# Optimization experiments

Measured on AMD Instinct MI355X. Metric: run time of the kernel, lower is better.

The kernel has to match this reference:

```python
import jax, jax.numpy as jnp
import numpy as np
import itertools

N_OBJECTS = 6  # subsets of range(6), sizes 1..6 -> 63 subsets

def _subset_groups():
    # group subsets by length so each group runs as one batched LSTM
    groups = {}
    for m in range(1, N_OBJECTS + 1):
        for s in itertools.combinations(range(6), m):
            groups.setdefault(m, []).append(list(s))
    return [(m, np.asarray(v, dtype=np.int32)) for m, v in groups.items()]

SUBSET_GROUPS = _subset_groups()


def _lstm_final_h(x, W_ih, W_hh, b_ih, b_hh):
    """x: [B,T,D] -> final hidden state [B,H]. PyTorch gate order i,f,g,o."""
    H = W_hh.shape[1]
    B = x.shape[0]
    # precompute input projections for all timesteps: [B,T,4H]
    xz = jnp.einsum('btd,gd->btg', x, W_ih) + b_ih + b_hh

    def step(carry, xt):
        h, c = carry
        z = xt + h @ W_hh.T
        i, f, g, o = jnp.split(z, 4, axis=-1)
        c = jax.nn.sigmoid(f) * c + jax.nn.sigmoid(i) * jnp.tanh(g)
        h = jax.nn.sigmoid(o) * jnp.tanh(c)
        return (h, c), None

    h0 = jnp.zeros((B, H), x.dtype)
    (h, _), _ = jax.lax.scan(step, (h0, h0), jnp.swapaxes(xz, 0, 1))
    return h


def setup_inputs() -> dict:
    key = jax.random.key(0)
    ks = jax.random.split(key, 10)
    D, H, FC, A = 16, 128, 256, 10
    mb = 8192
    s = lambda k, shape, fan: jax.random.normal(k, shape, jnp.float32) * (1.0 / np.sqrt(fan))
    return {
        'x_input': jax.random.normal(ks[0], (mb, 6, D), jnp.float32),
        'W_ih': s(ks[1], (4 * H, D), D),
        'W_hh': s(ks[2], (4 * H, H), H),
        'b_ih': jnp.zeros((4 * H,), jnp.float32),
        'b_hh': jnp.zeros((4 * H,), jnp.float32),
        'fc1_W': s(ks[3], (FC, H), H),
        'fc1_b': jnp.zeros((FC,), jnp.float32),
        'fc2_W': s(ks[4], (A, FC), FC),
        'fc2_b': jnp.zeros((A,), jnp.float32),
    }


def reference(x_input, W_ih, W_hh, b_ih, b_hh, fc1_W, fc1_b, fc2_W, fc2_b):
    mb = x_input.shape[0]
    H = W_hh.shape[1]
    hs = []
    # subsets of the same length are batched into one LSTM pass (fused form of
    # the original 63-iteration python loop); aggregation is permutation-invariant
    for m, idx in SUBSET_GROUPS:
        nL = idx.shape[0]
        xg = x_input[:, idx, :]                       # [mb, nL, m, D] gather
        xg = xg.reshape(mb * nL, m, x_input.shape[-1])
        h = _lstm_final_h(xg, W_ih, W_hh, b_ih, b_hh)  # [mb*nL, H]
        hs.append(h.reshape(mb, nL, H))
    holder = jnp.concatenate(hs, axis=1)              # [mb, 63, H]
    x = jnp.max(holder, axis=1)                       # aggregate == 'max'
    x = jax.nn.relu(x @ fc1_W.T + fc1_b)
    x = x @ fc2_W.T + fc2_b
    return jax.nn.log_softmax(x, axis=-1)
```

## Files before the change

kernel.cpp:

```cpp
#include <hip/hip_runtime.h>
#include <hip/hip_bf16.h>

#define BLOCK   512
#define NSAMP   32
#define HDIM    128
#define DDIM    16
#define NOBJ    6
#define NSLOT   16

typedef __attribute__((ext_vector_type(8))) short bf16x8;
typedef __attribute__((ext_vector_type(4))) float f32x4;

constexpr int pc6(int m)  { int c = 0; for (int i = 0; i < 6; ++i) c += (m >> i) & 1; return c; }
constexpr int msb6(int m) { int b = -1; for (int i = 0; i < 6; ++i) if (m & (1 << i)) b = i; return b; }

struct NodeRec { int jo, ps, sl; };
struct Plan { int cnt[7]; int n1[7]; NodeRec nd[7][20]; };
constexpr Plan make_plan() {
    Plan P{};
    int slotOf[64] = {};
    bool busy[NSLOT] = {};
    for (int d = 1; d <= 6; ++d) {
        int n = 0;
        for (int M = 1; M < 64; ++M) {
            if (pc6(M) != d || msb6(M) != 5) continue;
            P.nd[d][n].jo = 5;
            P.nd[d][n].ps = (d == 1) ? -1 : slotOf[M & ~(1 << 5)];
            P.nd[d][n].sl = -1;
            ++n;
        }
        int pend[20] = {}; int np = 0;
        for (int M = 1; M < 64; ++M) {
            if (pc6(M) != d || msb6(M) >= 5) continue;
            const int hi = msb6(M);
            int fs = -1;
            for (int s = 0; s < NSLOT; ++s) if (!busy[s]) { fs = s; break; }
            if (fs >= 0) {
                busy[fs] = true; slotOf[M] = fs;
                P.nd[d][n].jo = hi;
                P.nd[d][n].ps = (d == 1) ? -1 : slotOf[M & ~(1 << hi)];
                P.nd[d][n].sl = fs;
                ++n;
            } else pend[np++] = M;
        }
        P.n1[d] = n;
        int freeds[20] = {}; int nf = 0;
        if (d >= 2)
            for (int M = 1; M < 64; ++M)
                if (pc6(M) == d - 1 && msb6(M) == 4) freeds[nf++] = slotOf[M];
        for (int i = 0; i < np; ++i) {
            const int M = pend[i]; const int hi = msb6(M);
            const int s = freeds[--nf];
            slotOf[M] = s;
            P.nd[d][n].jo = hi;
            P.nd[d][n].ps = slotOf[M & ~(1 << hi)];
            P.nd[d][n].sl = s;
            ++n;
        }
        P.cnt[d] = n;
        for (int s = 0; s < NSLOT; ++s) busy[s] = false;
        for (int M = 1; M < 64; ++M)
            if (pc6(M) == d && msb6(M) < 5) busy[slotOf[M]] = true;
    }
    return P;
}
constexpr Plan PL = make_plan();

#define LOG2E   1.44269504f
#define TWOL2E  2.88539008f
#define SLOT_SH (16 * NSAMP * 8)

__device__ __forceinline__ float fast_sig(float z) {
    float e = __builtin_amdgcn_exp2f(-LOG2E * z);
    return __builtin_amdgcn_rcpf(1.0f + e);
}
__device__ __forceinline__ float fast_tanh(float z) {
    float e = __builtin_amdgcn_exp2f(TWOL2E * z);
    float r = __builtin_amdgcn_rcpf(1.0f + e);
    return fmaf(-2.0f, r, 1.0f);
}
__device__ __forceinline__ unsigned short f2bf(float x) {
    union { float f; unsigned int u; } a; a.f = x;
    unsigned int r = (a.u + 0x7FFFu + ((a.u >> 16) & 1u)) >> 16;
    return (unsigned short)r;
}
__device__ __forceinline__ unsigned pk2(float a, float b) {
    union { __hip_bfloat162 h; unsigned u; } z;
    z.h = __float22bfloat162_rn(float2{a, b});
    return z.u;
}
__device__ __forceinline__ float bflo(unsigned p) {
    union { unsigned u; float f; } a; a.u = p << 16; return a.f;
}
__device__ __forceinline__ float bfhi(unsigned p) {
    union { unsigned u; float f; } a; a.u = p & 0xFFFF0000u; return a.f;
}


__global__ __launch_bounds__(BLOCK, 2)
void subset_lstm_n32_kernel(
    const float* __restrict__ x_input,
    const float* __restrict__ W_ih,
    const float* __restrict__ W_hh,
    const float* __restrict__ b_ih,
    const float* __restrict__ b_hh,
    const float* __restrict__ fc1_W,
    const float* __restrict__ fc1_b,
    const float* __restrict__ fc2_W,
    const float* __restrict__ fc2_b,
    float* __restrict__ out)
{
    __shared__ __align__(16) unsigned short hs[NSLOT * SLOT_SH];
    __shared__ __align__(16) unsigned short xb[NOBJ * 2 * NSAMP * 8];
    __shared__ __align__(16) unsigned short xpad[16];
    float* s_maxh  = (float*)hs;
    float* s_fc1   = (float*)(hs + 8192);
    float* s_logit = (float*)xb;

    const int t      = threadIdx.x;
    const int w      = t >> 6;
    const int lane   = t & 63;
    const int quad   = lane >> 4;
    const int m16    = lane & 15;
    const int s_base = blockIdx.x * NSAMP;

    if (t < 16) xpad[t] = (t == 0) ? f2bf(1.0f) : (unsigned short)0;

    for (int idx = t; idx < NOBJ * 2 * NSAMP * 8; idx += BLOCK) {
        const int j = idx & 7, n = (idx >> 3) & 31, q = (idx >> 8) & 1, obj = idx >> 9;
        xb[idx] = f2bf(x_input[(s_base + n) * (NOBJ * DDIM) + obj * DDIM + q * 8 + j]);
    }

    bf16x8 wf[4][5];
    #pragma unroll
    for (int g = 0; g < 4; ++g) {
        const int grow = g * HDIM + w * 16 + m16;
        const float* whr = W_hh + grow * HDIM;
        const float* wir = W_ih + grow * DDIM;
        #pragma unroll
        for (int q = 0; q < 4; ++q) {
            union { unsigned short u[8]; bf16x8 v; } pk;
            #pragma unroll
            for (int j = 0; j < 8; ++j)
                pk.u[j] = f2bf(whr[q * 32 + quad * 8 + j]);
            wf[g][q] = pk.v;
        }
        {
            union { unsigned short u[8]; bf16x8 v; } pk;
            #pragma unroll
            for (int j = 0; j < 8; ++j) {
                float v = 0.0f;
                if (quad < 2) v = wir[quad * 8 + j];
                else if (quad == 2 && j == 0) v = b_ih[grow] + b_hh[grow];
                pk.u[j] = f2bf(v);
            }
            wf[g][4] = pk.v;
        }
    }

    uint2 cs[NSLOT][2];
    float mh[2][4];
    #pragma unroll
    for (int st = 0; st < 2; ++st)
        #pragma unroll
        for (int r = 0; r < 4; ++r) mh[st][r] = -1e30f;

    const int kslot = w * 2 + (quad >> 1);

    #pragma unroll
    for (int d = 1; d <= 6; ++d) {
        __syncthreads();
        #pragma unroll
        for (int ni = 0; ni < PL.cnt[d]; ++ni) {
            if (ni == PL.n1[d]) __syncthreads();
            const int jo = PL.nd[d][ni].jo;
            const int ps = PL.nd[d][ni].ps;
            const int sl = PL.nd[d][ni].sl;

            f32x4 acc[4][2];
            #pragma unroll
            for (int g = 0; g < 4; ++g)
                #pragma unroll
                for (int st = 0; st < 2; ++st)
                    acc[g][st] = f32x4{0.f, 0.f, 0.f, 0.f};

            #pragma unroll
            for (int st = 0; st < 2; ++st) {
                const unsigned short* bp = (quad < 2)
                    ? &xb[((jo * 2 + quad) * NSAMP + st * 16 + m16) * 8]
                    : &xpad[(quad - 2) * 8];
                const bf16x8 bfx = *(const bf16x8*)bp;
                #pragma unroll
                for (int g = 0; g < 4; ++g)
                    acc[g][st] = __builtin_amdgcn_mfma_f32_16x16x32_bf16(
                        wf[g][4], bfx, acc[g][st], 0, 0, 0);
            }
            if (ps >= 0) {
                #pragma unroll
                for (int q = 0; q < 4; ++q)
                    #pragma unroll
                    for (int st = 0; st < 2; ++st) {
                        const bf16x8 bh = *(const bf16x8*)
                            &hs[((ps * 16 + q * 4 + quad) * NSAMP + st * 16 + m16) * 8];
                        #pragma unroll
                        for (int g = 0; g < 4; ++g)
                            acc[g][st] = __builtin_amdgcn_mfma_f32_16x16x32_bf16(
                                wf[g][q], bh, acc[g][st], 0, 0, 0);
                    }
            }

            #pragma unroll
            for (int st = 0; st < 2; ++st) {
                float cn4[4], hn4[4];
                #pragma unroll
                for (int r = 0; r < 4; ++r) {
                    float cprev = 0.0f;
                    if (ps >= 0) {
                        const unsigned p = (r < 2) ? cs[ps][st].x : cs[ps][st].y;
                        cprev = (r & 1) ? bfhi(p) : bflo(p);
                    }
                    const float ig = fast_sig(acc[0][st][r]);
                    const float fg = fast_sig(acc[1][st][r]);
                    const float gg = fast_tanh(acc[2][st][r]);
                    const float og = fast_sig(acc[3][st][r]);
                    const float cn = fmaf(fg, cprev, ig * gg);
                    const float h  = og * fast_tanh(cn);
                    cn4[r] = cn; hn4[r] = h;
                    mh[st][r] = fmaxf(mh[st][r], h);
                }
                if (sl >= 0) {
                    cs[sl][st].x = pk2(cn4[0], cn4[1]);
                    cs[sl][st].y = pk2(cn4[2], cn4[3]);
                    union { __hip_bfloat162 h2[2]; uint2 v; } hp;
                    hp.h2[0] = __float22bfloat162_rn(float2{hn4[0], hn4[1]});
                    hp.h2[1] = __float22bfloat162_rn(float2{hn4[2], hn4[3]});
                    *(uint2*)&hs[((sl * 16 + kslot) * NSAMP + st * 16 + m16) * 8
                                 + (quad & 1) * 4] = hp.v;
                }
            }
        }
    }

    __syncthreads();
    #pragma unroll
    for (int st = 0; st < 2; ++st) {
        float4 v; v.x = mh[st][0]; v.y = mh[st][1]; v.z = mh[st][2]; v.w = mh[st][3];
        *(float4*)&s_maxh[(st * 16 + m16) * HDIM + w * 16 + quad * 4] = v;
    }
    __syncthreads();

    {
        const int f  = t & 255;
        const int sh = t >> 8;
        float a1[16];
        #pragma unroll
        for (int s = 0; s < 16; ++s) a1[s] = fc1_b[f];
        for (int k4 = 0; k4 < HDIM / 4; ++k4) {
            const float4 wv = *(const float4*)&fc1_W[f * HDIM + k4 * 4];
            #pragma unroll
            for (int s = 0; s < 16; ++s) {
                const float4 h4 = *(const float4*)&s_maxh[(sh * 16 + s) * HDIM + k4 * 4];
                a1[s] += wv.x * h4.x + wv.y * h4.y + wv.z * h4.z + wv.w * h4.w;
            }
        }
        #pragma unroll
        for (int s = 0; s < 16; ++s)
            s_fc1[(sh * 16 + s) * 256 + f] = fmaxf(a1[s], 0.0f);
    }
    __syncthreads();

    if (t < NSAMP * 10) {
        const int s = t / 10, a = t % 10;
        float acc2 = fc2_b[a];
        for (int f4 = 0; f4 < 256 / 4; ++f4) {
            const float4 wv = *(const float4*)&fc2_W[a * 256 + f4 * 4];
            const float4 v  = *(const float4*)&s_fc1[s * 256 + f4 * 4];
            acc2 += wv.x * v.x + wv.y * v.y + wv.z * v.z + wv.w * v.w;
        }
        s_logit[s * 10 + a] = acc2;
    }
    __syncthreads();

    if (t < NSAMP) {
        float m = -1e30f;
        #pragma unroll
        for (int a = 0; a < 10; ++a) m = fmaxf(m, s_logit[t * 10 + a]);
        float sum = 0.0f;
        #pragma unroll
        for (int a = 0; a < 10; ++a) sum += __expf(s_logit[t * 10 + a] - m);
        const float lse = m + __logf(sum);
        #pragma unroll
        for (int a = 0; a < 10; ++a)
            out[(s_base + t) * 10 + a] = s_logit[t * 10 + a] - lse;
    }
}

extern "C" void kernel_launch(void* const* d_in, const int* in_sizes, int n_in,
                              void* d_out, int out_size, void* d_ws, size_t ws_size,
                              hipStream_t stream)
{
    (void)d_ws; (void)ws_size; (void)n_in; (void)out_size;

    const float* x   = (const float*)d_in[0];
    const float* Wih = (const float*)d_in[1];
    const float* Whh = (const float*)d_in[2];
    const float* bih = (const float*)d_in[3];
    const float* bhh = (const float*)d_in[4];
    const float* f1w = (const float*)d_in[5];
    const float* f1b = (const float*)d_in[6];
    const float* f2w = (const float*)d_in[7];
    const float* f2b = (const float*)d_in[8];

    const int mb = in_sizes[0] / (NOBJ * DDIM);
    dim3 grid(mb / NSAMP), block(BLOCK);
    subset_lstm_n32_kernel<<<grid, block, 0, stream>>>(
        x, Wih, Whh, bih, bhh, f1w, f1b, f2w, f2b, (float*)d_out);
}
```

Baseline: 221.3 us.

## Halve samples per block, pair subset nodes, fold activation scales into weights

```diff
diff --git a/kernel.cpp b/kernel.cpp
--- a/kernel.cpp
+++ b/kernel.cpp
@@ -2,7 +2,7 @@
 #include <hip/hip_bf16.h>
 
 #define BLOCK   512
-#define NSAMP   32
+#define NSAMP   16
 #define HDIM    128
 #define DDIM    16
 #define NOBJ    6
@@ -70,15 +70,6 @@
 #define TWOL2E  2.88539008f
 #define SLOT_SH (16 * NSAMP * 8)
 
-__device__ __forceinline__ float fast_sig(float z) {
-    float e = __builtin_amdgcn_exp2f(-LOG2E * z);
-    return __builtin_amdgcn_rcpf(1.0f + e);
-}
-__device__ __forceinline__ float fast_tanh(float z) {
-    float e = __builtin_amdgcn_exp2f(TWOL2E * z);
-    float r = __builtin_amdgcn_rcpf(1.0f + e);
-    return fmaf(-2.0f, r, 1.0f);
-}
 __device__ __forceinline__ unsigned short f2bf(float x) {
     union { float f; unsigned int u; } a; a.f = x;
     unsigned int r = (a.u + 0x7FFFu + ((a.u >> 16) & 1u)) >> 16;
@@ -95,10 +86,18 @@
 __device__ __forceinline__ float bfhi(unsigned p) {
     union { unsigned u; float f; } a; a.u = p & 0xFFFF0000u; return a.f;
 }
-
-
-__global__ __launch_bounds__(BLOCK, 2)
-void subset_lstm_n32_kernel(
+__device__ __forceinline__ float sig_pre(float zp) {
+    return __builtin_amdgcn_rcpf(1.0f + __builtin_amdgcn_exp2f(zp));
+}
+__device__ __forceinline__ float tanh_pre(float zp) {
+    float r = __builtin_amdgcn_rcpf(1.0f + __builtin_amdgcn_exp2f(zp));
+    return fmaf(-2.0f, r, 1.0f);
+}
+
+
+__global__ __launch_bounds__(BLOCK)
+__attribute__((amdgpu_waves_per_eu(2, 2)))
+void subset_lstm_pair_kernel(
     const float* __restrict__ x_input,
     const float* __restrict__ W_ih,
     const float* __restrict__ W_hh,
@@ -114,7 +113,7 @@
     __shared__ __align__(16) unsigned short xb[NOBJ * 2 * NSAMP * 8];
     __shared__ __align__(16) unsigned short xpad[16];
     float* s_maxh  = (float*)hs;
-    float* s_fc1   = (float*)(hs + 8192);
+    float* s_fc1   = (float*)(hs + 4096);
     float* s_logit = (float*)xb;
 
     const int t      = threadIdx.x;
@@ -127,13 +126,14 @@
     if (t < 16) xpad[t] = (t == 0) ? f2bf(1.0f) : (unsigned short)0;
 
     for (int idx = t; idx < NOBJ * 2 * NSAMP * 8; idx += BLOCK) {
-        const int j = idx & 7, n = (idx >> 3) & 31, q = (idx >> 8) & 1, obj = idx >> 9;
+        const int j = idx & 7, n = (idx >> 3) & 15, q = (idx >> 7) & 1, obj = idx >> 8;
         xb[idx] = f2bf(x_input[(s_base + n) * (NOBJ * DDIM) + obj * DDIM + q * 8 + j]);
     }
 
     bf16x8 wf[4][5];
     #pragma unroll
     for (int g = 0; g < 4; ++g) {
+        const float sc = (g == 2) ? TWOL2E : -LOG2E;
         const int grow = g * HDIM + w * 16 + m16;
         const float* whr = W_hh + grow * HDIM;
         const float* wir = W_ih + grow * DDIM;
@@ -142,7 +142,7 @@
             union { unsigned short u[8]; bf16x8 v; } pk;
             #pragma unroll
             for (int j = 0; j < 8; ++j)
-                pk.u[j] = f2bf(whr[q * 32 + quad * 8 + j]);
+                pk.u[j] = f2bf(sc * whr[q * 32 + quad * 8 + j]);
             wf[g][q] = pk.v;
         }
         {
@@ -150,122 +150,119 @@
             #pragma unroll
             for (int j = 0; j < 8; ++j) {
                 float v = 0.0f;
-                if (quad < 2) v = wir[quad * 8 + j];
-                else if (quad == 2 && j == 0) v = b_ih[grow] + b_hh[grow];
+                if (quad < 2) v = sc * wir[quad * 8 + j];
+                else if (quad == 2 && j == 0) v = sc * (b_ih[grow] + b_hh[grow]);
                 pk.u[j] = f2bf(v);
             }
             wf[g][4] = pk.v;
         }
     }
 
-    uint2 cs[NSLOT][2];
-    float mh[2][4];
-    #pragma unroll
-    for (int st = 0; st < 2; ++st)
-        #pragma unroll
-        for (int r = 0; r < 4; ++r) mh[st][r] = -1e30f;
-
+    uint2 cs[NSLOT];
+    float mh[4] = {-1e30f, -1e30f, -1e30f, -1e30f};
     const int kslot = w * 2 + (quad >> 1);
 
     #pragma unroll
     for (int d = 1; d <= 6; ++d) {
         __syncthreads();
         #pragma unroll
-        for (int ni = 0; ni < PL.cnt[d]; ++ni) {
-            if (ni == PL.n1[d]) __syncthreads();
-            const int jo = PL.nd[d][ni].jo;
-            const int ps = PL.nd[d][ni].ps;
-            const int sl = PL.nd[d][ni].sl;
-
-            f32x4 acc[4][2];
+        for (int seg = 0; seg < 2; ++seg) {
+            const int sBeg = seg ? PL.n1[d] : 0;
+            const int sEnd = seg ? PL.cnt[d] : PL.n1[d];
+            if (seg && sBeg >= sEnd) continue;
+            if (seg) __syncthreads();
+
             #pragma unroll
-            for (int g = 0; g < 4; ++g)
+            for (int ni = sBeg; ni < sEnd; ni += 2) {
+                f32x4 acc[2][4];
                 #pragma unroll
-                for (int st = 0; st < 2; ++st)
-                    acc[g][st] = f32x4{0.f, 0.f, 0.f, 0.f};
-
-            #pragma unroll
-            for (int st = 0; st < 2; ++st) {
-                const unsigned short* bp = (quad < 2)
-                    ? &xb[((jo * 2 + quad) * NSAMP + st * 16 + m16) * 8]
-                    : &xpad[(quad - 2) * 8];
-                const bf16x8 bfx = *(const bf16x8*)bp;
+                for (int e = 0; e < 2; ++e) {
+                    if (ni + e >= sEnd) continue;
+                    const int jo = PL.nd[d][ni + e].jo;
+                    const int ps = PL.nd[d][ni + e].ps;
+                    #pragma unroll
+                    for (int g = 0; g < 4; ++g)
+                        acc[e][g] = f32x4{0.f, 0.f, 0.f, 0.f};
+                    const unsigned short* bp = (quad < 2)
+                        ? &xb[((jo * 2 + quad) * NSAMP + m16) * 8]
+                        : &xpad[(quad - 2) * 8];
+                    const bf16x8 bfx = *(const bf16x8*)bp;
+                    #pragma unroll
+                    for (int g = 0; g < 4; ++g)
+                        acc[e][g] = __builtin_amdgcn_mfma_f32_16x16x32_bf16(
+                            wf[g][4], bfx, acc[e][g], 0, 0, 0);
+                    if (ps >= 0) {
+                        #pragma unroll
+                        for (int q = 0; q < 4; ++q) {
+                            const bf16x8 bh = *(const bf16x8*)
+                                &hs[((ps * 16 + q * 4 + quad) * NSAMP + m16) * 8];
+                            #pragma unroll
+                            for (int g = 0; g < 4; ++g)
+                                acc[e][g] = __builtin_amdgcn_mfma_f32_16x16x32_bf16(
+                                    wf[g][q], bh, acc[e][g], 0, 0, 0);
+                        }
+                    }
+                }
                 #pragma unroll
-                for (int g = 0; g < 4; ++g)
-                    acc[g][st] = __builtin_amdgcn_mfma_f32_16x16x32_bf16(
-                        wf[g][4], bfx, acc[g][st], 0, 0, 0);
-            }
-            if (ps >= 0) {
-                #pragma unroll
-                for (int q = 0; q < 4; ++q)
+                for (int e = 0; e < 2; ++e) {
+                    if (ni + e >= sEnd) continue;
+                    const int ps = PL.nd[d][ni + e].ps;
+                    const int sl = PL.nd[d][ni + e].sl;
+                    float cn4[4], hn4[4];
                     #pragma unroll
-                    for (int st = 0; st < 2; ++st) {
-                        const bf16x8 bh = *(const bf16x8*)
-                            &hs[((ps * 16 + q * 4 + quad) * NSAMP + st * 16 + m16) * 8];
-                        #pragma unroll
-                        for (int g = 0; g < 4; ++g)
-                            acc[g][st] = __builtin_amdgcn_mfma_f32_16x16x32_bf16(
-                                wf[g][q], bh, acc[g][st], 0, 0, 0);
+                    for (int r = 0; r < 4; ++r) {
+                        float cprev = 0.0f;
+                        if (ps >= 0) {
+                            const unsigned p = (r < 2) ? cs[ps].x : cs[ps].y;
+                            cprev = (r & 1) ? bfhi(p) : bflo(p);
+                        }
+                        const float ig = sig_pre(acc[e][0][r]);
+                        const float fg = sig_pre(acc[e][1][r]);
+                        const float gg = tanh_pre(acc[e][2][r]);
+                        const float og = sig_pre(acc[e][3][r]);
+                        const float cn = fmaf(fg, cprev, ig * gg);
+                        const float h  = og * tanh_pre(TWOL2E * cn);
+                        cn4[r] = cn; hn4[r] = h;
+                        mh[r] = fmaxf(mh[r], h);
                     }
-            }
-
-            #pragma unroll
-            for (int st = 0; st < 2; ++st) {
-                float cn4[4], hn4[4];
-                #pragma unroll
-                for (int r = 0; r < 4; ++r) {
-                    float cprev = 0.0f;
-                    if (ps >= 0) {
-                        const unsigned p = (r < 2) ? cs[ps][st].x : cs[ps][st].y;
-                        cprev = (r & 1) ? bfhi(p) : bflo(p);
+                    if (sl >= 0) {
+                        cs[sl].x = pk2(cn4[0], cn4[1]);
+                        cs[sl].y = pk2(cn4[2], cn4[3]);
+                        union { __hip_bfloat162 h2[2]; uint2 v; } hp;
+                        hp.h2[0] = __float22bfloat162_rn(float2{hn4[0], hn4[1]});
+                        hp.h2[1] = __float22bfloat162_rn(float2{hn4[2], hn4[3]});
+                        *(uint2*)&hs[((sl * 16 + kslot) * NSAMP + m16) * 8
+                                     + (quad & 1) * 4] = hp.v;
                     }
-                    const float ig = fast_sig(acc[0][st][r]);
-                    const float fg = fast_sig(acc[1][st][r]);
-                    const float gg = fast_tanh(acc[2][st][r]);
-                    const float og = fast_sig(acc[3][st][r]);
-                    const float cn = fmaf(fg, cprev, ig * gg);
-                    const float h  = og * fast_tanh(cn);
-                    cn4[r] = cn; hn4[r] = h;
-                    mh[st][r] = fmaxf(mh[st][r], h);
-                }
-                if (sl >= 0) {
-                    cs[sl][st].x = pk2(cn4[0], cn4[1]);
-                    cs[sl][st].y = pk2(cn4[2], cn4[3]);
-                    union { __hip_bfloat162 h2[2]; uint2 v; } hp;
-                    hp.h2[0] = __float22bfloat162_rn(float2{hn4[0], hn4[1]});
-                    hp.h2[1] = __float22bfloat162_rn(float2{hn4[2], hn4[3]});
-                    *(uint2*)&hs[((sl * 16 + kslot) * NSAMP + st * 16 + m16) * 8
-                                 + (quad & 1) * 4] = hp.v;
                 }
             }
         }
     }
 
     __syncthreads();
-    #pragma unroll
-    for (int st = 0; st < 2; ++st) {
-        float4 v; v.x = mh[st][0]; v.y = mh[st][1]; v.z = mh[st][2]; v.w = mh[st][3];
-        *(float4*)&s_maxh[(st * 16 + m16) * HDIM + w * 16 + quad * 4] = v;
+    {
+        float4 v; v.x = mh[0]; v.y = mh[1]; v.z = mh[2]; v.w = mh[3];
+        *(float4*)&s_maxh[m16 * HDIM + w * 16 + quad * 4] = v;
     }
     __syncthreads();
 
     {
         const int f  = t & 255;
         const int sh = t >> 8;
-        float a1[16];
-        #pragma unroll
-        for (int s = 0; s < 16; ++s) a1[s] = fc1_b[f];
+        float a1[8];
+        #pragma unroll
+        for (int s = 0; s < 8; ++s) a1[s] = fc1_b[f];
         for (int k4 = 0; k4 < HDIM / 4; ++k4) {
             const float4 wv = *(const float4*)&fc1_W[f * HDIM + k4 * 4];
             #pragma unroll
-            for (int s = 0; s < 16; ++s) {
-                const float4 h4 = *(const float4*)&s_maxh[(sh * 16 + s) * HDIM + k4 * 4];
+            for (int s = 0; s < 8; ++s) {
+                const float4 h4 = *(const float4*)&s_maxh[(sh * 8 + s) * HDIM + k4 * 4];
                 a1[s] += wv.x * h4.x + wv.y * h4.y + wv.z * h4.z + wv.w * h4.w;
             }
         }
         #pragma unroll
-        for (int s = 0; s < 16; ++s)
-            s_fc1[(sh * 16 + s) * 256 + f] = fmaxf(a1[s], 0.0f);
+        for (int s = 0; s < 8; ++s)
+            s_fc1[(sh * 8 + s) * 256 + f] = fmaxf(a1[s], 0.0f);
     }
     __syncthreads();
 
@@ -313,6 +310,6 @@
 
     const int mb = in_sizes[0] / (NOBJ * DDIM);
     dim3 grid(mb / NSAMP), block(BLOCK);
-    subset_lstm_n32_kernel<<<grid, block, 0, stream>>>(
+    subset_lstm_pair_kernel<<<grid, block, 0, stream>>>(
         x, Wih, Whh, bih, bhh, f1w, f1b, f2w, f2b, (float*)d_out);
 }
```

After: 207.5 us. 1.07x faster.
